# Optimization experiments

Measured on AMD Instinct MI355X. Metric: run time of the kernel, lower is better.

Reference implementation:

```python
import jax, jax.numpy as jnp
import numpy as np

ENT_GRID = 16
ENT_DIM = 64
N_RELATION = 5000
EMB_DIM = ENT_GRID * ENT_DIM  # 1024
BATCH = 8192
LN_EPS = 1e-5


def setup_inputs() -> dict:
    key = jax.random.key(0)
    k1, k2, k3, k4 = jax.random.split(key, 4)
    ent_emb = jax.random.normal(k1, (BATCH, EMB_DIM), dtype=jnp.float32)
    proj_ids = jax.random.randint(k2, (BATCH,), 0, N_RELATION, dtype=jnp.int64)
    # xavier_uniform for relation_tran: fan_in = fan_out treated over last two dims
    lim_t = float(np.sqrt(6.0 / (ENT_GRID + ENT_GRID)))
    relation_tran = jax.random.uniform(
        k3, (N_RELATION, ENT_DIM, ENT_GRID, ENT_GRID), jnp.float32, -lim_t, lim_t)
    lim_b = float(np.sqrt(6.0 / (ENT_DIM + ENT_GRID)))
    relation_bias = jax.random.uniform(
        k4, (N_RELATION, ENT_DIM, ENT_GRID), jnp.float32, -lim_b, lim_b)
    ln_weight = jnp.ones((EMB_DIM,), dtype=jnp.float32)
    ln_bias = jnp.zeros((EMB_DIM,), dtype=jnp.float32)
    return {
        "ent_emb": ent_emb,
        "proj_ids": proj_ids,
        "relation_tran": relation_tran,
        "relation_bias": relation_bias,
        "ln_weight": ln_weight,
        "ln_bias": ln_bias,
    }


def _layer_norm(x, w, b, eps=LN_EPS):
    mu = jnp.mean(x, axis=-1, keepdims=True)
    var = jnp.mean(jnp.square(x - mu), axis=-1, keepdims=True)
    return (x - mu) * jax.lax.rsqrt(var + eps) * w + b


def reference(ent_emb, proj_ids, relation_tran, relation_bias, ln_weight, ln_bias):
    B = ent_emb.shape[0]
    # gather per-query relation transform and bias
    rel_tran = relation_tran[proj_ids]  # (B, ent_dim, g, g)
    rel_bias = relation_bias[proj_ids]  # (B, ent_dim, g)
    # distribute: (B, emb_dim) -> (B, ent_dim, ent_grid); torch.chunk+stack == contiguous reshape
    e = ent_emb.reshape(B, ENT_DIM, ENT_GRID)
    # batched small matmul: (g,g) @ (g,) per (batch, ent_dim) block, plus bias
    x = jnp.einsum('bdgh,bdh->bdg', rel_tran, e) + rel_bias
    out = _layer_norm(x.reshape(B, EMB_DIM), ln_weight, ln_bias)
    return out
```

## Files before the change

kernel.cpp:

```cpp
#include <hip/hip_runtime.h>

#define ENT_GRID 16
#define ENT_DIM  64
#define EMB      1024
#define LN_EPS   1e-5f

__global__ __launch_bounds__(256, 4)
void wproj_ln_kernel(const float* __restrict__ ent_emb,
                     const int*   __restrict__ proj_ids,
                     const float* __restrict__ rel_tran,
                     const float* __restrict__ rel_bias,
                     const float* __restrict__ ln_w,
                     const float* __restrict__ ln_b,
                     float* __restrict__ out) {
    const int b = blockIdx.x;
    const int t = threadIdx.x;

    const long long r = (long long)proj_ids[b];
    const float* __restrict__ tran = rel_tran + (size_t)r * (ENT_DIM * ENT_GRID * ENT_GRID);
    const float* __restrict__ bias = rel_bias + (size_t)r * (ENT_DIM * ENT_GRID);
    const float* __restrict__ e    = ent_emb  + (size_t)b * EMB;

    __shared__ float se[EMB];
    __shared__ float wsum[4], wsq[4];

    reinterpret_cast<float4*>(se)[t] = reinterpret_cast<const float4*>(e)[t];
    __syncthreads();

    float x[4];
    float sum = 0.0f, sumsq = 0.0f;

#pragma unroll
    for (int k = 0; k < 4; ++k) {
        const int i = t + k * 256;
        const int d = i >> 4;
        const float4* __restrict__ tr = reinterpret_cast<const float4*>(tran + (size_t)i * ENT_GRID);
        const float4* __restrict__ er = reinterpret_cast<const float4*>(se + d * ENT_GRID);
        float acc = bias[i];
#pragma unroll
        for (int q = 0; q < 4; ++q) {
            float4 a  = tr[q];
            float4 ev = er[q];
            acc += a.x * ev.x + a.y * ev.y + a.z * ev.z + a.w * ev.w;
        }
        x[k]  = acc;
        sum   += acc;
        sumsq += acc * acc;
    }

#pragma unroll
    for (int off = 32; off > 0; off >>= 1) {
        sum   += __shfl_xor(sum, off, 64);
        sumsq += __shfl_xor(sumsq, off, 64);
    }
    const int wid = t >> 6;
    if ((t & 63) == 0) { wsum[wid] = sum; wsq[wid] = sumsq; }
    __syncthreads();

    const float tsum = wsum[0] + wsum[1] + wsum[2] + wsum[3];
    const float tsq  = wsq[0]  + wsq[1]  + wsq[2]  + wsq[3];
    const float mu   = tsum * (1.0f / (float)EMB);
    const float var  = tsq * (1.0f / (float)EMB) - mu * mu;
    const float rstd = rsqrtf(var + LN_EPS);

    float* __restrict__ ob = out + (size_t)b * EMB;
#pragma unroll
    for (int k = 0; k < 4; ++k) {
        const int i = t + k * 256;
        ob[i] = (x[k] - mu) * rstd * ln_w[i] + ln_b[i];
    }
}

extern "C" void kernel_launch(void* const* d_in, const int* in_sizes, int n_in,
                              void* d_out, int out_size, void* d_ws, size_t ws_size,
                              hipStream_t stream) {
    const float* ent_emb  = (const float*)d_in[0];
    const int*   proj_ids = (const int*)  d_in[1];
    const float* rel_tran = (const float*)d_in[2];
    const float* rel_bias = (const float*)d_in[3];
    const float* ln_w     = (const float*)d_in[4];
    const float* ln_b     = (const float*)d_in[5];
    float* out = (float*)d_out;

    const int B = in_sizes[1];

    wproj_ln_kernel<<<B, 256, 0, stream>>>(ent_emb, proj_ids, rel_tran, rel_bias,
                                           ln_w, ln_b, out);
}
```

Baseline: 91.67 us.

## Counting-sort batch rows by relation id and swizzle blocks across XCDs for L2 reuse

Adds a histogram, scan and scatter pre-pass that builds a permutation grouping batch rows by relation id. The main kernel processes rows in that order. Block ids are remapped so consecutive sorted rows land on the same XCD, letting rows that share a relation reuse its 64KB transform from that XCD's L2 instead of refetching it from HBM. The cost is four extra small kernel launches, including a single-block serial scan, plus atomics in the workspace.

```diff
diff --git a/kernel.cpp b/kernel.cpp
--- a/kernel.cpp
+++ b/kernel.cpp
@@ -4,16 +4,74 @@
 #define ENT_DIM  64
 #define EMB      1024
 #define LN_EPS   1e-5f
+#define NXCD     8
+
+
+__global__ void zero_hist_kernel(int* __restrict__ hist, int n) {
+    int i = blockIdx.x * blockDim.x + threadIdx.x;
+    if (i < n) hist[i] = 0;
+}
+
+__global__ void hist_kernel(const int* __restrict__ ids, int* __restrict__ hist, int B) {
+    int i = blockIdx.x * blockDim.x + threadIdx.x;
+    if (i < B) atomicAdd(&hist[ids[i]], 1);
+}
+
+__global__ __launch_bounds__(1024)
+void scan_kernel(const int* __restrict__ hist, int* __restrict__ cursor, int n) {
+    const int t = threadIdx.x;
+    const int ITEMS = (n + 1023) / 1024;
+    int vals[8];
+    int lsum = 0;
+#pragma unroll
+    for (int k = 0; k < 8; ++k) {
+        int i = t * ITEMS + k;
+        int v = (k < ITEMS && i < n) ? hist[i] : 0;
+        vals[k] = v;
+        lsum += v;
+    }
+    __shared__ int s[1024];
+    s[t] = lsum;
+    __syncthreads();
+    for (int off = 1; off < 1024; off <<= 1) {
+        int v = (t >= off) ? s[t - off] : 0;
+        __syncthreads();
+        s[t] += v;
+        __syncthreads();
+    }
+    int run = s[t] - lsum;
+#pragma unroll
+    for (int k = 0; k < 8; ++k) {
+        int i = t * ITEMS + k;
+        if (k < ITEMS && i < n) cursor[i] = run;
+        run += vals[k];
+    }
+}
+
+__global__ void scatter_kernel(const int* __restrict__ ids, int* __restrict__ cursor,
+                               int* __restrict__ perm, int B) {
+    int i = blockIdx.x * blockDim.x + threadIdx.x;
+    if (i < B) {
+        int pos = atomicAdd(&cursor[ids[i]], 1);
+        perm[pos] = i;
+    }
+}
 
 __global__ __launch_bounds__(256, 4)
 void wproj_ln_kernel(const float* __restrict__ ent_emb,
-                     const int*   __restrict__ proj_ids,
                      const float* __restrict__ rel_tran,
                      const float* __restrict__ rel_bias,
                      const float* __restrict__ ln_w,
                      const float* __restrict__ ln_b,
-                     float* __restrict__ out) {
-    const int b = blockIdx.x;
+                     const int*   __restrict__ proj_ids,
+                     const int*   __restrict__ perm,
+                     float* __restrict__ out,
+                     int nblk_per_xcd, int use_swizzle) {
+    int g = blockIdx.x;
+    if (use_swizzle) {
+        g = (g % NXCD) * nblk_per_xcd + g / NXCD;
+    }
+    const int b = perm[g];
     const int t = threadIdx.x;
 
     const long long r = (long long)proj_ids[b];
@@ -82,8 +140,20 @@
     const float* ln_b     = (const float*)d_in[5];
     float* out = (float*)d_out;
 
-    const int B = in_sizes[1];
+    const int B  = in_sizes[1];
+    const int NR = in_sizes[2] / (ENT_DIM * ENT_GRID * ENT_GRID);
 
-    wproj_ln_kernel<<<B, 256, 0, stream>>>(ent_emb, proj_ids, rel_tran, rel_bias,
-                                           ln_w, ln_b, out);
+    int* w      = (int*)d_ws;
+    int* hist   = w;
+    int* cursor = w + NR;
+    int* perm   = w + 2 * NR;
+
+    zero_hist_kernel<<<(NR + 255) / 256, 256, 0, stream>>>(hist, NR);
+    hist_kernel<<<(B + 255) / 256, 256, 0, stream>>>(proj_ids, hist, B);
+    scan_kernel<<<1, 1024, 0, stream>>>(hist, cursor, NR);
+    scatter_kernel<<<(B + 255) / 256, 256, 0, stream>>>(proj_ids, cursor, perm, B);
+
+    const int use_swizzle = (B % NXCD == 0) ? 1 : 0;
+    wproj_ln_kernel<<<B, 256, 0, stream>>>(ent_emb, rel_tran, rel_bias, ln_w, ln_b,
+                                           proj_ids, perm, out, B / NXCD, use_swizzle);
 }
```

After: 95.74 us. +4.4%, slower.
